# Kernel optimization log

Hardware: AMD Instinct MI355X
Metric: run time of the kernel (lower is better)

Reference implementation:

```python
import jax, jax.numpy as jnp
import numpy as np

B, NFIELD = 8192, 20
NFEAT = 100000
SQL_VOCAB = NFIELD + NFEAT + 1  # 100021
SQL_NEMB, DATA_NEMB = 16, 64
HID = 1024
OUT = 1
K = 16
ALPHA = 1.5
N_BISECT = 50


def entmax_bisect(x, alpha=ALPHA, n_iter=N_BISECT):
    # alpha-entmax via bisection on the threshold tau (Peters et al. 2019).
    am1 = alpha - 1.0
    x = x * am1
    d = x.shape[-1]
    max_val = jnp.max(x, axis=-1, keepdims=True)
    tau_lo = max_val - 1.0
    tau_hi = max_val - d ** (1.0 - alpha)

    def p(tau):
        return jnp.clip(x - tau, 0.0) ** (1.0 / am1)

    f_lo = jnp.sum(p(tau_lo), axis=-1, keepdims=True) - 1.0

    def body(carry, _):
        tau_lo, tau_hi, f_lo = carry
        tau_m = 0.5 * (tau_lo + tau_hi)
        f_m = jnp.sum(p(tau_m), axis=-1, keepdims=True) - 1.0
        same_side = (f_m * f_lo) >= 0
        tau_lo = jnp.where(same_side, tau_m, tau_lo)
        tau_hi = jnp.where(same_side, tau_hi, tau_m)
        f_lo = jnp.where(same_side, f_m, f_lo)
        return (tau_lo, tau_hi, f_lo), None

    (tau_lo, tau_hi, _), _ = jax.lax.scan(body, (tau_lo, tau_hi, f_lo), None, length=n_iter)
    pm = p(0.5 * (tau_lo + tau_hi))
    return pm / jnp.sum(pm, axis=-1, keepdims=True)


def cv_squared(v):
    eps = 1e-10
    var = jnp.var(v, ddof=1)  # torch .var() is unbiased
    mean = jnp.mean(v)
    return var / (mean * mean + eps)


def setup_inputs() -> dict:
    key = jax.random.key(0)
    ks = jax.random.split(key, 12)
    xavier = lambda k, shp: jax.random.uniform(k, shp, jnp.float32, -1.0, 1.0) * jnp.sqrt(6.0 / (shp[-2] + shp[-1]))
    inp = {
        "x": jax.random.randint(ks[0], (B, NFIELD), 0, NFEAT),
        "sql": jax.random.randint(ks[1], (B, NFIELD), 0, SQL_VOCAB),
        "sql_emb_table": xavier(ks[2], (SQL_VOCAB, SQL_NEMB)),
        "input_emb_table": xavier(ks[3], (NFEAT, DATA_NEMB)),
        # gate: Linear(gate_in, HID) -> ReLU -> Linear(HID, K)
        "gW1": xavier(ks[4], (NFIELD * SQL_NEMB, HID)),
        "gb1": jnp.zeros((HID,), jnp.float32),
        "gW2": xavier(ks[5], (HID, K)),
        "gb2": jnp.zeros((K,), jnp.float32),
        # K experts: Linear(in, HID) -> ReLU -> Linear(HID, OUT), stacked on axis 0
        "eW1": xavier(ks[6], (K, NFIELD * DATA_NEMB, HID)),
        "eb1": jnp.zeros((K, HID), jnp.float32),
        "eW2": xavier(ks[7], (K, HID, OUT)),
        "eb2": jnp.zeros((K, OUT), jnp.float32),
    }
    return inp


def reference(x, sql, sql_emb_table, input_emb_table, gW1, gb1, gW2, gb2, eW1, eb1, eW2, eb2):
    Bn = x.shape[0]
    x_emb = input_emb_table[x].reshape(Bn, -1)      # [B, nfield*data_nemb]
    sql_emb = sql_emb_table[sql].reshape(Bn, -1)    # [B, nfield*sql_nemb]

    # gate network + entmax-bisect (dropout is identity in eval)
    g = jax.nn.relu(sql_emb @ gW1 + gb1) @ gW2 + gb2  # [B, K]
    gate_score = entmax_bisect(g)                     # [B, K], sparse simplex

    loss = cv_squared(jnp.sum(gate_score, axis=0))

    # all K experts on every token, vectorized
    h = jax.nn.relu(jnp.einsum("bi,kih->bkh", x_emb, eW1) + eb1)  # [B, K, HID]
    y_k = jnp.einsum("bkh,kho->bko", h, eW2) + eb2                # [B, K, OUT]
    y = jnp.sum(gate_score[:, :, None] * y_k, axis=1)             # [B, OUT]
    return (y.squeeze(-1), loss)
```

## Files before the change

kernel.cpp:

```cpp
#include <hip/hip_runtime.h>
#include <stdint.h>

#define NFIELD 20
#define HID 1024
#define KEXP 16
#define KX 1280
#define KS 320
#define BATCH 8192

typedef __bf16 bf16x8 __attribute__((ext_vector_type(8)));
typedef float f32x4 __attribute__((ext_vector_type(4)));

__device__ __forceinline__ unsigned short f2bf(float f) {
  union { float f; unsigned u; } v; v.f = f;
  unsigned r = v.u + 0x7FFFu + ((v.u >> 16) & 1u);
  return (unsigned short)(r >> 16);
}

__device__ __forceinline__ void gload16(const void* g, void* l) {
  __builtin_amdgcn_global_load_lds(
      (const __attribute__((address_space(1))) unsigned int*)(uintptr_t)g,
      (__attribute__((address_space(3))) unsigned int*)(unsigned)(uintptr_t)l,
      16, 0, 0);
}

#define SBAR() asm volatile("s_barrier" ::: "memory")


__global__ void transpose_cvt(const float* __restrict__ src, unsigned short* __restrict__ dst,
                              int R, int C, long sstride, long dstride) {
  __shared__ float tile[32][33];
  const float* s = src + (size_t)blockIdx.z * sstride;
  unsigned short* d = dst + (size_t)blockIdx.z * dstride;
  const int r0 = blockIdx.y * 32, c0 = blockIdx.x * 32;
  const int tx = threadIdx.x & 31, ty = threadIdx.x >> 5;
#pragma unroll
  for (int i = 0; i < 4; ++i)
    tile[ty + 8 * i][tx] = s[(size_t)(r0 + ty + 8 * i) * C + c0 + tx];
  __syncthreads();
#pragma unroll
  for (int i = 0; i < 4; ++i)
    d[(size_t)(c0 + ty + 8 * i) * R + r0 + tx] = f2bf(tile[tx][ty + 8 * i]);
}

__global__ void gather_x_k(const int* __restrict__ x, const float* __restrict__ tab,
                           unsigned short* __restrict__ out) {
  const int b = blockIdx.x;
  const int f = threadIdx.x >> 4;
  const int q = threadIdx.x & 15;
  const int idx = x[b * NFIELD + f];
  const float4 v = *(const float4*)(tab + (size_t)idx * 64 + q * 4);
  ushort4 o;
  o.x = f2bf(v.x); o.y = f2bf(v.y); o.z = f2bf(v.z); o.w = f2bf(v.w);
  *(ushort4*)(out + (size_t)b * KX + f * 64 + q * 4) = o;
}

__global__ void gather_sql_k(const int* __restrict__ sql, const float* __restrict__ tab,
                             unsigned short* __restrict__ out) {
  const int t = blockIdx.x * 256 + threadIdx.x;
  const int b = t / 80;
  const int r = t - b * 80;
  const int f = r >> 2, q = r & 3;
  const int idx = sql[b * NFIELD + f];
  const float4 v = *(const float4*)(tab + (size_t)idx * 16 + q * 4);
  ushort4 o;
  o.x = f2bf(v.x); o.y = f2bf(v.y); o.z = f2bf(v.z); o.w = f2bf(v.w);
  *(ushort4*)(out + (size_t)b * KS + f * 16 + q * 4) = o;
}

template <int NJO, int KTOT>
__global__ __launch_bounds__(256, 2) void gemm_k(const __bf16* __restrict__ A,
                                                 const __bf16* __restrict__ Bt,
                                                 const float* __restrict__ bias,
                                                 const float* __restrict__ W2,
                                                 float* __restrict__ out) {
  constexpr int NT = KTOT / 64;
  alignas(16) __shared__ __bf16 As[2][128][64];
  alignas(16) __shared__ __bf16 Bs[2][128][64];

  const int tid = threadIdx.x;
  const int lane = tid & 63;
  const int wave = tid >> 6;
  const int wr = wave >> 1;
  const int wc = wave & 1;

  const unsigned f = blockIdx.y * gridDim.x + blockIdx.x;
  const unsigned nwg = gridDim.x * gridDim.y;
  const unsigned s = (f >> 3) + (f & 7u) * (nwg >> 3);
  const int m0 = (int)((s & 511u) >> 3) * 128;
  const int n0 = (int)((s >> 9) * 8 + (s & 7u)) * 128;

  const int srow = lane >> 3;
  const int sch = (lane & 7) ^ srow;
  const int r15 = lane & 15, g4 = lane >> 4;

  const __bf16* Ag = A + (size_t)(m0 + wave * 32 + srow) * KTOT + sch * 8;
  const __bf16* Bg = Bt + (size_t)(n0 + wave * 32 + srow) * KTOT + sch * 8;

  auto stage = [&](int t) {
    const int c = t & 1;
#pragma unroll
    for (int j = 0; j < 4; ++j)
      gload16(Ag + (size_t)(j * 8) * KTOT + t * 64, (void*)&As[c][wave * 32 + j * 8][0]);
#pragma unroll
    for (int j = 0; j < 4; ++j)
      gload16(Bg + (size_t)(j * 8) * KTOT + t * 64, (void*)&Bs[c][wave * 32 + j * 8][0]);
  };

  f32x4 acc[4][4] = {};

  stage(0);
  if (NT > 1) { stage(1); asm volatile("s_waitcnt vmcnt(8)" ::: "memory"); }
  else        {           asm volatile("s_waitcnt vmcnt(0)" ::: "memory"); }
  SBAR();

#pragma unroll 2
  for (int t = 0; t < NT; ++t) {
    const int c = t & 1;
    bf16x8 af[4][2], bfr[4][2];
#pragma unroll
    for (int mi = 0; mi < 4; ++mi) {
      const int row = wr * 64 + mi * 16 + r15;
#pragma unroll
      for (int kk = 0; kk < 2; ++kk)
        af[mi][kk] = *(const bf16x8*)&As[c][row][((kk * 4 + g4) ^ (row & 7)) * 8];
    }
#pragma unroll
    for (int ni = 0; ni < 4; ++ni) {
      const int row = wc * 64 + ni * 16 + r15;
#pragma unroll
      for (int kk = 0; kk < 2; ++kk)
        bfr[ni][kk] = *(const bf16x8*)&Bs[c][row][((kk * 4 + g4) ^ (row & 7)) * 8];
    }
    __builtin_amdgcn_s_setprio(1);
#pragma unroll
    for (int mi = 0; mi < 4; ++mi)
#pragma unroll
      for (int ni = 0; ni < 4; ++ni)
        acc[mi][ni] = __builtin_amdgcn_mfma_f32_16x16x32_bf16(af[mi][0], bfr[ni][0], acc[mi][ni], 0, 0, 0);
    __builtin_amdgcn_s_setprio(0);
    SBAR();
    if (t + 2 < NT) stage(t + 2);
    __builtin_amdgcn_s_setprio(1);
#pragma unroll
    for (int mi = 0; mi < 4; ++mi)
#pragma unroll
      for (int ni = 0; ni < 4; ++ni)
        acc[mi][ni] = __builtin_amdgcn_mfma_f32_16x16x32_bf16(af[mi][1], bfr[ni][1], acc[mi][ni], 0, 0, 0);
    __builtin_amdgcn_s_setprio(0);
    if (t + 2 < NT) asm volatile("s_waitcnt vmcnt(8)" ::: "memory");
    else            asm volatile("s_waitcnt vmcnt(0)" ::: "memory");
    SBAR();
  }

  int ncol[4];
  float bsv[4];
#pragma unroll
  for (int ni = 0; ni < 4; ++ni) {
    ncol[ni] = n0 + wc * 64 + ni * 16 + r15;
    bsv[ni] = bias[ncol[ni]];
  }
#pragma unroll
  for (int mi = 0; mi < 4; ++mi)
#pragma unroll
    for (int ni = 0; ni < 4; ++ni)
#pragma unroll
      for (int j = 0; j < 4; ++j) {
        float v = acc[mi][ni][j] + bsv[ni];
        acc[mi][ni][j] = v > 0.f ? v : 0.f;
      }
#pragma unroll
  for (int jo = 0; jo < NJO; ++jo) {
    float w4[4];
#pragma unroll
    for (int ni = 0; ni < 4; ++ni)
      w4[ni] = (NJO == 1) ? W2[ncol[ni]] : W2[ncol[ni] * NJO + jo];
#pragma unroll
    for (int mi = 0; mi < 4; ++mi)
#pragma unroll
      for (int j = 0; j < 4; ++j) {
        float s = acc[mi][0][j] * w4[0] + acc[mi][1][j] * w4[1] +
                  acc[mi][2][j] * w4[2] + acc[mi][3][j] * w4[3];
        s += __shfl_xor(s, 1);
        s += __shfl_xor(s, 2);
        s += __shfl_xor(s, 4);
        s += __shfl_xor(s, 8);
        if (r15 == 0) {
          const int row = m0 + wr * 64 + mi * 16 + g4 * 4 + j;
          const int oc = (NJO == 1) ? (n0 >> 10) : jo;
          atomicAdd(&out[row * KEXP + oc], s);
        }
      }
  }
}

__global__ void entmax_combine(const float* __restrict__ gacc, const float* __restrict__ gb2,
                               const float* __restrict__ yk, const float* __restrict__ eb2,
                               float* __restrict__ y, double* __restrict__ colsum) {
  const int b = blockIdx.x * 256 + threadIdx.x;
  float x[16];
  float mx = -3.4e38f;
#pragma unroll
  for (int j = 0; j < 16; ++j) {
    x[j] = (gacc[b * 16 + j] + gb2[j]) * 0.5f;
    mx = fmaxf(mx, x[j]);
  }
  float lo = mx - 1.0f, hi = mx - 0.25f;
  float flo = -1.0f;
#pragma unroll
  for (int j = 0; j < 16; ++j) {
    float d = x[j] - lo; d = d > 0.f ? d : 0.f;
    flo += d * d;
  }
  for (int it = 0; it < 50; ++it) {
    const float tm = 0.5f * (lo + hi);
    float fm = -1.0f;
#pragma unroll
    for (int j = 0; j < 16; ++j) {
      float d = x[j] - tm; d = d > 0.f ? d : 0.f;
      fm += d * d;
    }
    if (fm * flo >= 0.f) { lo = tm; flo = fm; } else { hi = tm; }
  }
  const float tm = 0.5f * (lo + hi);
  float p[16], ps = 0.f;
#pragma unroll
  for (int j = 0; j < 16; ++j) {
    float d = x[j] - tm; d = d > 0.f ? d : 0.f;
    p[j] = d * d; ps += p[j];
  }
  const float inv = 1.0f / ps;
  float yv = 0.f;
#pragma unroll
  for (int j = 0; j < 16; ++j) {
    p[j] *= inv;
    yv += p[j] * (yk[b * 16 + j] + eb2[j]);
  }
  y[b] = yv;

  const int lane = threadIdx.x & 63, wv = threadIdx.x >> 6;
  __shared__ float red[4][16];
#pragma unroll
  for (int j = 0; j < 16; ++j) {
    float v = p[j];
    v += __shfl_xor(v, 1);  v += __shfl_xor(v, 2);  v += __shfl_xor(v, 4);
    v += __shfl_xor(v, 8);  v += __shfl_xor(v, 16); v += __shfl_xor(v, 32);
    if (lane == 0) red[wv][j] = v;
  }
  __syncthreads();
  if (threadIdx.x < 16) {
    double s = (double)red[0][threadIdx.x] + (double)red[1][threadIdx.x] +
               (double)red[2][threadIdx.x] + (double)red[3][threadIdx.x];
    atomicAdd(&colsum[threadIdx.x], s);
  }
}

__global__ void loss_k(const double* __restrict__ colsum, float* __restrict__ out) {
  if (threadIdx.x == 0 && blockIdx.x == 0) {
    double m = 0.0;
    for (int k = 0; k < 16; ++k) m += colsum[k];
    m *= (1.0 / 16.0);
    double var = 0.0;
    for (int k = 0; k < 16; ++k) { const double d = colsum[k] - m; var += d * d; }
    var *= (1.0 / 15.0);
    out[0] = (float)(var / (m * m + 1e-10));
  }
}

extern "C" void kernel_launch(void* const* d_in, const int* in_sizes, int n_in,
                              void* d_out, int out_size, void* d_ws, size_t ws_size,
                              hipStream_t stream) {
  const int*   x    = (const int*)d_in[0];
  const int*   sql  = (const int*)d_in[1];
  const float* sqlT = (const float*)d_in[2];
  const float* inT  = (const float*)d_in[3];
  const float* gW1  = (const float*)d_in[4];
  const float* gb1  = (const float*)d_in[5];
  const float* gW2  = (const float*)d_in[6];
  const float* gb2  = (const float*)d_in[7];
  const float* eW1  = (const float*)d_in[8];
  const float* eb1  = (const float*)d_in[9];
  const float* eW2  = (const float*)d_in[10];
  const float* eb2  = (const float*)d_in[11];

  char* ws = (char*)d_ws;
  unsigned short* eW1T = (unsigned short*)(ws);
  unsigned short* xemb = (unsigned short*)(ws + 41943040);
  unsigned short* semb = (unsigned short*)(ws + 62914560);
  unsigned short* gW1T = (unsigned short*)(ws + 68157440);
  float*  yk     = (float*)(ws + 68812800);
  float*  gacc   = (float*)(ws + 69337088);
  double* colsum = (double*)(ws + 69861376);

  hipMemsetAsync(yk, 0, 524288 * 2 + 128, stream);

  transpose_cvt<<<dim3(32, 40, 16), 256, 0, stream>>>(eW1, eW1T, 1280, 1024, 1280L * 1024, 1024L * 1280);
  transpose_cvt<<<dim3(32, 10, 1), 256, 0, stream>>>(gW1, gW1T, 320, 1024, 0, 0);
  gather_x_k<<<BATCH, 320, 0, stream>>>(x, inT, xemb);
  gather_sql_k<<<BATCH * 80 / 256, 256, 0, stream>>>(sql, sqlT, semb);

  gemm_k<1, KX><<<dim3(16384 / 128, BATCH / 128), 256, 0, stream>>>(
      (const __bf16*)xemb, (const __bf16*)eW1T, eb1, eW2, yk);
  gemm_k<16, KS><<<dim3(HID / 128, BATCH / 128), 256, 0, stream>>>(
      (const __bf16*)semb, (const __bf16*)gW1T, gb1, gW2, gacc);

  entmax_combine<<<BATCH / 256, 256, 0, stream>>>(gacc, gb2, yk, eb2, (float*)d_out, colsum);
  loss_k<<<1, 64, 0, stream>>>(colsum, (float*)d_out + BATCH);
}
```

Before: 517.9 us.

## Use 256x256 tile, 8-wave GEMM with interleaved staging for expert layer

Adds a new 512-thread GEMM kernel with 256x256 output tiles for the large expert first-layer GEMM, replacing the 128x128 tile kernel. Loads are split into half-tile stages interleaved with MFMA quadrants under barriers and raised priority, so global-to-LDS loads overlap compute. The larger tile halves global traffic per FLOP, at the cost of 128KB of LDS, more registers and lower occupancy. The fused bias, ReLU, W2-dot and atomic epilogue is kept.

```diff
diff --git a/kernel.cpp b/kernel.cpp
--- a/kernel.cpp
+++ b/kernel.cpp
@@ -68,6 +68,176 @@
   *(ushort4*)(out + (size_t)b * KS + f * 16 + q * 4) = o;
 }
 
+template <int KTOT>
+__global__ __launch_bounds__(512, 2) void gemm256(const __bf16* __restrict__ A,
+                                                  const __bf16* __restrict__ Bt,
+                                                  const float* __restrict__ bias,
+                                                  const float* __restrict__ W2,
+                                                  float* __restrict__ out) {
+  constexpr int NT = KTOT / 64;
+  static_assert(NT % 2 == 0 && NT >= 4, "even NT only");
+  alignas(16) __shared__ __bf16 As[2][256][64];
+  alignas(16) __shared__ __bf16 Bs[2][256][64];
+
+  const int tid = threadIdx.x;
+  const int lane = tid & 63;
+  const int wave = tid >> 6;
+  const int wr = wave >> 2;
+  const int wc = wave & 3;
+
+  const unsigned f = blockIdx.y * gridDim.x + blockIdx.x;
+  const unsigned c8 = f >> 3;
+  const int n0 = (int)((f & 7u) * 8 + (c8 & 7u)) * 256;
+  const int m0 = (int)(c8 >> 3) * 256;
+
+  const int srow = lane >> 3;
+  const int sch = (lane & 7) ^ srow;
+  const int r15 = lane & 15, g4 = lane >> 4;
+
+  const __bf16* Ag = A + (size_t)(m0 + srow) * KTOT + sch * 8;
+  const __bf16* Bg = Bt + (size_t)(n0 + srow) * KTOT + sch * 8;
+  const int k2 = wave * 2;
+
+  auto stA = [&](int t, int mh) {
+    if (t >= NT) return;
+    __bf16* base = &As[t & 1][0][0];
+#pragma unroll
+    for (int j = 0; j < 2; ++j) {
+      const int k = k2 + j;
+      const int r = ((k >> 3) << 7) + mh * 64 + (k & 7) * 8;
+      gload16(Ag + (size_t)r * KTOT + t * 64, (void*)(base + r * 64));
+    }
+  };
+  auto stB = [&](int t, int nh) {
+    if (t >= NT) return;
+    __bf16* base = &Bs[t & 1][0][0];
+#pragma unroll
+    for (int j = 0; j < 2; ++j) {
+      const int k = k2 + j;
+      const int r = (k >> 2) * 64 + nh * 32 + (k & 3) * 8;
+      gload16(Bg + (size_t)r * KTOT + t * 64, (void*)(base + r * 64));
+    }
+  };
+  auto rdA = [&](int c, int mh, bf16x8 (&af)[4][2]) {
+#pragma unroll
+    for (int mi = 0; mi < 4; ++mi) {
+      const int row = wr * 128 + mh * 64 + mi * 16 + r15;
+#pragma unroll
+      for (int kk = 0; kk < 2; ++kk)
+        af[mi][kk] = *(const bf16x8*)&As[c][row][((kk * 4 + g4) ^ (row & 7)) * 8];
+    }
+  };
+  auto rdB = [&](int c, int nh, bf16x8 (&bb)[2][2]) {
+#pragma unroll
+    for (int ni = 0; ni < 2; ++ni) {
+      const int row = wc * 64 + nh * 32 + ni * 16 + r15;
+#pragma unroll
+      for (int kk = 0; kk < 2; ++kk)
+        bb[ni][kk] = *(const bf16x8*)&Bs[c][row][((kk * 4 + g4) ^ (row & 7)) * 8];
+    }
+  };
+
+  f32x4 acc[8][4] = {};
+  bf16x8 af[4][2], b0[2][2], b1[2][2];
+
+#define MM(AF, BB, MH, NH)                                                        \
+  __builtin_amdgcn_s_setprio(1);                                                  \
+  _Pragma("unroll") for (int mi = 0; mi < 4; ++mi)                                \
+  _Pragma("unroll") for (int ni = 0; ni < 2; ++ni)                                \
+  _Pragma("unroll") for (int kk = 0; kk < 2; ++kk)                                \
+      acc[(MH)*4 + mi][(NH)*2 + ni] = __builtin_amdgcn_mfma_f32_16x16x32_bf16(    \
+          AF[mi][kk], BB[ni][kk], acc[(MH)*4 + mi][(NH)*2 + ni], 0, 0, 0);        \
+  __builtin_amdgcn_s_setprio(0);
+
+  stA(0, 0); stB(0, 0); stB(0, 1); stA(0, 1);
+  stA(1, 0); stB(1, 0); stB(1, 1);
+  asm volatile("s_waitcnt vmcnt(6)" ::: "memory");
+  SBAR();
+
+  for (int i = 0; i < NT / 2; ++i) {
+    const int t0 = 2 * i, t1 = 2 * i + 1;
+    rdA(0, 0, af); rdB(0, 0, b0);
+    stA(t1, 1);
+    SBAR(); __builtin_amdgcn_sched_barrier(0);
+    MM(af, b0, 0, 0);
+    SBAR();
+    rdB(0, 1, b1);
+    stA(t0 + 2, 0);
+    SBAR(); __builtin_amdgcn_sched_barrier(0);
+    MM(af, b1, 0, 1);
+    SBAR();
+    rdA(0, 1, af);
+    stB(t0 + 2, 0);
+    SBAR(); __builtin_amdgcn_sched_barrier(0);
+    MM(af, b1, 1, 1);
+    SBAR();
+    stB(t0 + 2, 1);
+    SBAR(); __builtin_amdgcn_sched_barrier(0);
+    MM(af, b0, 1, 0);
+    if (t0 + 2 < NT) asm volatile("s_waitcnt vmcnt(6)" ::: "memory");
+    else             asm volatile("s_waitcnt vmcnt(0)" ::: "memory");
+    SBAR();
+    rdA(1, 0, af); rdB(1, 0, b0);
+    stA(t0 + 2, 1);
+    SBAR(); __builtin_amdgcn_sched_barrier(0);
+    MM(af, b0, 0, 0);
+    SBAR();
+    rdB(1, 1, b1);
+    stA(t1 + 2, 0);
+    SBAR(); __builtin_amdgcn_sched_barrier(0);
+    MM(af, b1, 0, 1);
+    SBAR();
+    rdA(1, 1, af);
+    stB(t1 + 2, 0);
+    SBAR(); __builtin_amdgcn_sched_barrier(0);
+    MM(af, b1, 1, 1);
+    SBAR();
+    stB(t1 + 2, 1);
+    SBAR(); __builtin_amdgcn_sched_barrier(0);
+    MM(af, b0, 1, 0);
+    if (t1 + 2 < NT) asm volatile("s_waitcnt vmcnt(6)" ::: "memory");
+    else             asm volatile("s_waitcnt vmcnt(0)" ::: "memory");
+    SBAR();
+  }
+#undef MM
+
+  int ncol[4];
+  float bsv[4];
+#pragma unroll
+  for (int b = 0; b < 4; ++b) {
+    ncol[b] = n0 + wc * 64 + (b >> 1) * 32 + (b & 1) * 16 + r15;
+    bsv[b] = bias[ncol[b]];
+  }
+#pragma unroll
+  for (int a = 0; a < 8; ++a)
+#pragma unroll
+    for (int b = 0; b < 4; ++b)
+#pragma unroll
+      for (int j = 0; j < 4; ++j) {
+        float v = acc[a][b][j] + bsv[b];
+        acc[a][b][j] = v > 0.f ? v : 0.f;
+      }
+  float w4[4];
+#pragma unroll
+  for (int b = 0; b < 4; ++b) w4[b] = W2[ncol[b]];
+  const int oc = n0 >> 10;
+#pragma unroll
+  for (int a = 0; a < 8; ++a)
+#pragma unroll
+    for (int j = 0; j < 4; ++j) {
+      float s = acc[a][0][j] * w4[0] + acc[a][1][j] * w4[1] +
+                acc[a][2][j] * w4[2] + acc[a][3][j] * w4[3];
+      s += __shfl_xor(s, 1);
+      s += __shfl_xor(s, 2);
+      s += __shfl_xor(s, 4);
+      s += __shfl_xor(s, 8);
+      if (r15 == 0) {
+        const int row = m0 + wr * 128 + (a >> 2) * 64 + (a & 3) * 16 + g4 * 4 + j;
+        atomicAdd(&out[row * KEXP + oc], s);
+      }
+    }
+}
+
 template <int NJO, int KTOT>
 __global__ __launch_bounds__(256, 2) void gemm_k(const __bf16* __restrict__ A,
                                                  const __bf16* __restrict__ Bt,
@@ -81,8 +251,7 @@
   const int tid = threadIdx.x;
   const int lane = tid & 63;
   const int wave = tid >> 6;
-  const int wr = wave >> 1;
-  const int wc = wave & 1;
+  const int wr = wave >> 1, wc = wave & 1;
 
   const unsigned f = blockIdx.y * gridDim.x + blockIdx.x;
   const unsigned nwg = gridDim.x * gridDim.y;
@@ -299,7 +468,7 @@
   gather_x_k<<<BATCH, 320, 0, stream>>>(x, inT, xemb);
   gather_sql_k<<<BATCH * 80 / 256, 256, 0, stream>>>(sql, sqlT, semb);
 
-  gemm_k<1, KX><<<dim3(16384 / 128, BATCH / 128), 256, 0, stream>>>(
+  gemm256<KX><<<dim3(16384 / 256, BATCH / 256), 512, 0, stream>>>(
       (const __bf16*)xemb, (const __bf16*)eW1T, eb1, eW2, yk);
   gemm_k<16, KS><<<dim3(HID / 128, BATCH / 128), 256, 0, stream>>>(
       (const __bf16*)semb, (const __bf16*)gW1T, gb1, gW2, gacc);
```

Result: no change. 515.7 us (-0.4%).

## Use producer-consumer warp specialization for the expert GEMM

Applied to the files above, without the earlier changes.

Adds a gemm_pc kernel with a fifth wave that only issues global-to-LDS loads, while four waves do the MFMA work. The expert GEMM launch switches to it with 320 threads. The aim is to overlap memory loads with matrix compute so that compute waves no longer issue loads. In exchange, the launch bounds drop the explicit two-blocks-per-CU hint and add an extra barrier per k-step, which may reduce occupancy.

```diff
diff --git a/kernel.cpp b/kernel.cpp
--- a/kernel.cpp
+++ b/kernel.cpp
@@ -68,6 +68,140 @@
   *(ushort4*)(out + (size_t)b * KS + f * 16 + q * 4) = o;
 }
 
+template <int KTOT>
+__global__ __launch_bounds__(320) void gemm_pc(const __bf16* __restrict__ A,
+                                               const __bf16* __restrict__ Bt,
+                                               const float* __restrict__ bias,
+                                               const float* __restrict__ W2,
+                                               float* __restrict__ out) {
+  constexpr int NT = KTOT / 64;
+  alignas(16) __shared__ __bf16 As[2][128][64];
+  alignas(16) __shared__ __bf16 Bs[2][128][64];
+
+  const int tid = threadIdx.x;
+  const int lane = tid & 63;
+  const int wave = tid >> 6;
+  const int wr = wave >> 1;
+  const int wc = wave & 1;
+
+  const unsigned f = blockIdx.y * gridDim.x + blockIdx.x;
+  const unsigned nwg = gridDim.x * gridDim.y;
+  const unsigned s = (f >> 3) + (f & 7u) * (nwg >> 3);
+  const int m0 = (int)((s & 511u) >> 3) * 128;
+  const int n0 = (int)((s >> 9) * 8 + (s & 7u)) * 128;
+
+  const int srow = lane >> 3;
+  const int sch = (lane & 7) ^ srow;
+  const int r15 = lane & 15, g4 = lane >> 4;
+
+  const __bf16* Ag = A + (size_t)(m0 + srow) * KTOT + sch * 8;
+  const __bf16* Bg = Bt + (size_t)(n0 + srow) * KTOT + sch * 8;
+
+  auto stage = [&](int t) {
+    const int c = t & 1;
+#pragma unroll
+    for (int j = 0; j < 16; ++j)
+      gload16(Ag + (size_t)(j * 8) * KTOT + t * 64, (void*)&As[c][j * 8][0]);
+#pragma unroll
+    for (int j = 0; j < 16; ++j)
+      gload16(Bg + (size_t)(j * 8) * KTOT + t * 64, (void*)&Bs[c][j * 8][0]);
+  };
+
+  f32x4 acc[4][4] = {};
+
+  if (wave == 4) {
+    stage(0);
+    if (NT > 1) stage(1);
+    asm volatile("s_waitcnt vmcnt(32)" ::: "memory");
+  }
+  SBAR();
+
+#pragma unroll 2
+  for (int t = 0; t < NT; ++t) {
+    const int c = t & 1;
+    bf16x8 af[4][2], bfr[4][2];
+    if (wave < 4) {
+#pragma unroll
+      for (int mi = 0; mi < 4; ++mi) {
+        const int row = wr * 64 + mi * 16 + r15;
+#pragma unroll
+        for (int kk = 0; kk < 2; ++kk)
+          af[mi][kk] = *(const bf16x8*)&As[c][row][((kk * 4 + g4) ^ (row & 7)) * 8];
+      }
+#pragma unroll
+      for (int ni = 0; ni < 4; ++ni) {
+        const int row = wc * 64 + ni * 16 + r15;
+#pragma unroll
+        for (int kk = 0; kk < 2; ++kk)
+          bfr[ni][kk] = *(const bf16x8*)&Bs[c][row][((kk * 4 + g4) ^ (row & 7)) * 8];
+      }
+      __builtin_amdgcn_s_setprio(1);
+#pragma unroll
+      for (int mi = 0; mi < 4; ++mi)
+#pragma unroll
+        for (int ni = 0; ni < 4; ++ni)
+          acc[mi][ni] = __builtin_amdgcn_mfma_f32_16x16x32_bf16(af[mi][0], bfr[ni][0], acc[mi][ni], 0, 0, 0);
+      __builtin_amdgcn_s_setprio(0);
+    }
+    SBAR();
+    if (wave < 4) {
+      __builtin_amdgcn_s_setprio(1);
+#pragma unroll
+      for (int mi = 0; mi < 4; ++mi)
+#pragma unroll
+        for (int ni = 0; ni < 4; ++ni)
+          acc[mi][ni] = __builtin_amdgcn_mfma_f32_16x16x32_bf16(af[mi][1], bfr[ni][1], acc[mi][ni], 0, 0, 0);
+      __builtin_amdgcn_s_setprio(0);
+    } else {
+      if (t + 2 < NT) {
+        stage(t + 2);
+        asm volatile("s_waitcnt vmcnt(32)" ::: "memory");
+      } else if (t + 1 < NT) {
+        asm volatile("s_waitcnt vmcnt(0)" ::: "memory");
+      }
+    }
+    SBAR();
+  }
+
+  if (wave == 4) return;
+
+  int ncol[4];
+  float bsv[4];
+#pragma unroll
+  for (int ni = 0; ni < 4; ++ni) {
+    ncol[ni] = n0 + wc * 64 + ni * 16 + r15;
+    bsv[ni] = bias[ncol[ni]];
+  }
+#pragma unroll
+  for (int mi = 0; mi < 4; ++mi)
+#pragma unroll
+    for (int ni = 0; ni < 4; ++ni)
+#pragma unroll
+      for (int j = 0; j < 4; ++j) {
+        float v = acc[mi][ni][j] + bsv[ni];
+        acc[mi][ni][j] = v > 0.f ? v : 0.f;
+      }
+  float w4[4];
+#pragma unroll
+  for (int ni = 0; ni < 4; ++ni) w4[ni] = W2[ncol[ni]];
+  const int oc = n0 >> 10;
+#pragma unroll
+  for (int mi = 0; mi < 4; ++mi)
+#pragma unroll
+    for (int j = 0; j < 4; ++j) {
+      float s = acc[mi][0][j] * w4[0] + acc[mi][1][j] * w4[1] +
+                acc[mi][2][j] * w4[2] + acc[mi][3][j] * w4[3];
+      s += __shfl_xor(s, 1);
+      s += __shfl_xor(s, 2);
+      s += __shfl_xor(s, 4);
+      s += __shfl_xor(s, 8);
+      if (r15 == 0) {
+        const int row = m0 + wr * 64 + mi * 16 + g4 * 4 + j;
+        atomicAdd(&out[row * KEXP + oc], s);
+      }
+    }
+}
+
 template <int NJO, int KTOT>
 __global__ __launch_bounds__(256, 2) void gemm_k(const __bf16* __restrict__ A,
                                                  const __bf16* __restrict__ Bt,
@@ -81,8 +215,7 @@
   const int tid = threadIdx.x;
   const int lane = tid & 63;
   const int wave = tid >> 6;
-  const int wr = wave >> 1;
-  const int wc = wave & 1;
+  const int wr = wave >> 1, wc = wave & 1;
 
   const unsigned f = blockIdx.y * gridDim.x + blockIdx.x;
   const unsigned nwg = gridDim.x * gridDim.y;
@@ -299,7 +432,7 @@
   gather_x_k<<<BATCH, 320, 0, stream>>>(x, inT, xemb);
   gather_sql_k<<<BATCH * 80 / 256, 256, 0, stream>>>(sql, sqlT, semb);
 
-  gemm_k<1, KX><<<dim3(16384 / 128, BATCH / 128), 256, 0, stream>>>(
+  gemm_pc<KX><<<dim3(16384 / 128, BATCH / 128), 320, 0, stream>>>(
       (const __bf16*)xemb, (const __bf16*)eW1T, eb1, eW2, yk);
   gemm_k<16, KS><<<dim3(HID / 128, BATCH / 128), 256, 0, stream>>>(
       (const __bf16*)semb, (const __bf16*)gW1T, gb1, gW2, gacc);
```

After: 610.4 us. 1.18x slower.

## Double-buffer MFMA fragments in registers to overlap LDS reads with compute

Applied to the files above, without the earlier changes.

Restructures the GEMM main loop so the next tile's A and B fragments are read from LDS into a second register set while the second half of the current tile's MFMAs runs. The loop is manually unrolled by two with alternating fragment buffers, and the tail is handled separately for odd and even tile counts. The intent is to hide LDS read latency behind matrix-core work. In exchange it raises register pressure and replaces the partial vmcnt(8) wait with a full vmcnt(0) plus lgkmcnt(0) each iteration, which may expose more global-load latency.

```diff
diff --git a/kernel.cpp b/kernel.cpp
--- a/kernel.cpp
+++ b/kernel.cpp
@@ -75,6 +75,7 @@
                                                  const float* __restrict__ W2,
                                                  float* __restrict__ out) {
   constexpr int NT = KTOT / 64;
+  static_assert(NT >= 3, "pipeline needs NT>=3");
   alignas(16) __shared__ __bf16 As[2][128][64];
   alignas(16) __shared__ __bf16 Bs[2][128][64];
 
@@ -106,18 +107,7 @@
     for (int j = 0; j < 4; ++j)
       gload16(Bg + (size_t)(j * 8) * KTOT + t * 64, (void*)&Bs[c][wave * 32 + j * 8][0]);
   };
-
-  f32x4 acc[4][4] = {};
-
-  stage(0);
-  if (NT > 1) { stage(1); asm volatile("s_waitcnt vmcnt(8)" ::: "memory"); }
-  else        {           asm volatile("s_waitcnt vmcnt(0)" ::: "memory"); }
-  SBAR();
-
-#pragma unroll 2
-  for (int t = 0; t < NT; ++t) {
-    const int c = t & 1;
-    bf16x8 af[4][2], bfr[4][2];
+  auto readfr = [&](int c, bf16x8 (&af)[4][2], bf16x8 (&bfr)[4][2]) {
 #pragma unroll
     for (int mi = 0; mi < 4; ++mi) {
       const int row = wr * 64 + mi * 16 + r15;
@@ -132,26 +122,50 @@
       for (int kk = 0; kk < 2; ++kk)
         bfr[ni][kk] = *(const bf16x8*)&Bs[c][row][((kk * 4 + g4) ^ (row & 7)) * 8];
     }
-    __builtin_amdgcn_s_setprio(1);
-#pragma unroll
-    for (int mi = 0; mi < 4; ++mi)
-#pragma unroll
-      for (int ni = 0; ni < 4; ++ni)
-        acc[mi][ni] = __builtin_amdgcn_mfma_f32_16x16x32_bf16(af[mi][0], bfr[ni][0], acc[mi][ni], 0, 0, 0);
-    __builtin_amdgcn_s_setprio(0);
-    SBAR();
-    if (t + 2 < NT) stage(t + 2);
-    __builtin_amdgcn_s_setprio(1);
-#pragma unroll
-    for (int mi = 0; mi < 4; ++mi)
-#pragma unroll
-      for (int ni = 0; ni < 4; ++ni)
-        acc[mi][ni] = __builtin_amdgcn_mfma_f32_16x16x32_bf16(af[mi][1], bfr[ni][1], acc[mi][ni], 0, 0, 0);
-    __builtin_amdgcn_s_setprio(0);
-    if (t + 2 < NT) asm volatile("s_waitcnt vmcnt(8)" ::: "memory");
-    else            asm volatile("s_waitcnt vmcnt(0)" ::: "memory");
-    SBAR();
-  }
+  };
+
+  f32x4 acc[4][4] = {};
+  bf16x8 afA[4][2], bfA[4][2], afB[4][2], bfB[4][2];
+
+#define MFMA16(AF, BF, KK)                                                     \
+  __builtin_amdgcn_s_setprio(1);                                               \
+  _Pragma("unroll") for (int mi = 0; mi < 4; ++mi)                             \
+  _Pragma("unroll") for (int ni = 0; ni < 4; ++ni)                             \
+      acc[mi][ni] = __builtin_amdgcn_mfma_f32_16x16x32_bf16(                   \
+          AF[mi][KK], BF[ni][KK], acc[mi][ni], 0, 0, 0);                       \
+  __builtin_amdgcn_s_setprio(0);
+
+#define BODY(T, AFC, BFC, AFN, BFN)                                            \
+  MFMA16(AFC, BFC, 0);                                                         \
+  asm volatile("s_waitcnt lgkmcnt(0)" ::: "memory");                           \
+  asm volatile("s_waitcnt vmcnt(0)" ::: "memory");                             \
+  SBAR();                                                                      \
+  if ((T) + 2 < NT) stage((T) + 2);                                            \
+  readfr(((T) + 1) & 1, AFN, BFN);                                             \
+  MFMA16(AFC, BFC, 1);                                                         \
+  SBAR();
+
+  stage(0);
+  stage(1);
+  asm volatile("s_waitcnt vmcnt(0)" ::: "memory");
+  SBAR();
+  readfr(0, afA, bfA);
+
+  int t = 0;
+  for (; t + 1 < NT - 1; t += 2) {
+    BODY(t, afA, bfA, afB, bfB);
+    BODY(t + 1, afB, bfB, afA, bfA);
+  }
+  if constexpr (((NT - 1) & 1) != 0) {
+    BODY(NT - 2, afA, bfA, afB, bfB);
+    MFMA16(afB, bfB, 0);
+    MFMA16(afB, bfB, 1);
+  } else {
+    MFMA16(afA, bfA, 0);
+    MFMA16(afA, bfA, 1);
+  }
+#undef BODY
+#undef MFMA16
 
   int ncol[4];
   float bsv[4];
```

Result: faster. 506.7 us (-2.2%).
